# Kernel tuning notes

Hardware: AMD Instinct MI355X
Metric: run time of the kernel (lower is better)

The kernel has to match this reference:

```python
import jax, jax.numpy as jnp
import numpy as np

# Reference for Net.get_seed_aff_x4 (+ Sinkhorn), the custom-kernel hotspot of this
# module. The ResNet50 conv stack / side convs are standard cuDNN-covered ops and the
# external `resnet50` module is not part of this source; `feature` here is hie_fea
# (768ch at side3 resolution) and `norm_cam` is the bg-augmented CAM at the same
# resolution, exactly as they arrive at get_seed_aff_x4 in forward.

N, C, H, W, CF = 8, 21, 64, 64, 768
NUM_CLUSTERS = 2
KMEANS_ITERS = 10      # deterministic Lloyd iterations (external kmeans_pytorch is
                       # randomly initialized; we use first-two-valid-pixel init)
EPS_OT = 0.1
SINK_MAX_ITER = 100
SINK_THRESH = 0.01


def setup_inputs() -> dict:
    key = jax.random.key(0)
    k1, k2, k3 = jax.random.split(key, 3)
    norm_cam = jax.random.uniform(k1, (N, C, H, W), dtype=jnp.float32)
    label = (jax.random.uniform(k2, (N, C, 1, 1)) < 0.8).astype(jnp.float32)
    label = label.at[:, 0].set(1.0)  # background always present
    feature = jax.random.normal(k3, (N, CF, H, W), dtype=jnp.float32)
    return {"norm_cam": norm_cam, "label": label, "feature": feature}


def _kmeans_cosine(feat, feat_n, mask):
    # feat: [HW, CF] raw features, feat_n: [HW, CF] l2-normalized, mask: [HW] in {0,1}
    valid = mask > 0
    cnt = valid.sum()
    order = jnp.argsort(jnp.where(valid, 0, 1))  # stable: valid pixels first
    init = feat[order[:NUM_CLUSTERS]] * mask[order[:NUM_CLUSTERS], None]

    def step(centers, _):
        cn = centers / jnp.maximum(
            jnp.linalg.norm(centers, axis=-1, keepdims=True), 1e-8)
        sim = feat_n @ cn.T                                  # [HW, K]
        assign = jnp.argmax(sim, axis=-1)
        oh = jax.nn.one_hot(assign, NUM_CLUSTERS, dtype=feat.dtype) * mask[:, None]
        counts = oh.sum(0)
        new_c = (oh.T @ feat) / jnp.maximum(counts, 1.0)[:, None]
        return new_c, None

    centers, _ = jax.lax.scan(step, init, None, length=KMEANS_ITERS)
    # original `continue` when < num_clusters valid pixels -> centers stay zero
    return jnp.where(cnt >= NUM_CLUSTERS, centers, jnp.zeros_like(centers))


def _sinkhorn(K, u, v):
    # K: [C, M, Nk]; faithful to Net.Sinkhorn incl. early stop on mean |r - r0|
    def cond(state):
        i, r, c, err = state
        return (i < SINK_MAX_ITER) & (err >= SINK_THRESH)

    def body(state):
        i, r, c, _ = state
        r0 = r
        r = u / jnp.einsum('cmk,ck->cm', K, c)
        c = v / jnp.einsum('cmk,cm->ck', K, r)
        err = jnp.abs(r - r0).mean()
        return (i + 1, r, c, err)

    state0 = (jnp.int32(0), jnp.ones_like(u), jnp.ones_like(v),
              jnp.asarray(jnp.inf, u.dtype))
    _, r, c, _ = jax.lax.while_loop(cond, body, state0)
    return r[..., None] * c[..., None, :] * K


def reference(norm_cam, label, feature):
    n, c, h, w = norm_cam.shape
    cf = feature.shape[1]
    hw = h * w

    # seeds: one-hot argmax of norm_cam, gated by image-level labels
    belonging = jnp.argmax(norm_cam, axis=1)                       # [n,h,w]
    seeds = jnp.transpose(jax.nn.one_hot(belonging, c, dtype=norm_cam.dtype),
                          (0, 3, 1, 2)) * label                    # [n,c,h,w]
    # nearest-interp to feature size is identity (same HxW by construction)
    mask = seeds.reshape(n, c, hw)                                 # [n,c,hw]

    feat = feature.reshape(n, cf, hw).transpose(0, 2, 1)           # [n,hw,cf]
    feat_n = feat / jnp.maximum(
        jnp.linalg.norm(feat, axis=-1, keepdims=True), 1e-8)

    # per-(image, class) cosine k-means, fully vectorized (no python data loops)
    centers = jax.vmap(
        lambda f, fn, ms: jax.vmap(_kmeans_cosine, in_axes=(None, None, 0))(f, fn, ms)
    )(feat, feat_n, mask)                                          # [n,c,K,cf]
    cnt = (mask > 0).sum(-1)                                       # [n,c]

    # cosine similarity of ALL pixels to the 2 centers, mean over clusters
    centers_n = centers / jnp.maximum(
        jnp.linalg.norm(centers, axis=-1, keepdims=True), 1e-8)
    cos = jnp.einsum('nmd,nckd->nckm', feat_n, centers_n)          # [n,c,K,hw]
    cam = jnp.where((cnt >= NUM_CLUSTERS)[..., None],
                    cos.mean(axis=2), 0.0).reshape(n, c, h, w)

    # --- Sinkhorn OT refinement (torch.no_grad in original) ---
    feat_ot = feat / (jnp.linalg.norm(feat, axis=-1, keepdims=True) + 1e-5)
    cflat = centers.reshape(n, c * NUM_CLUSTERS, cf)
    cflat = cflat / (jnp.linalg.norm(cflat, axis=-1, keepdims=True) + 1e-5)
    sim = jnp.einsum('nmd,njd->nmj', feat_ot, cflat)               # [n,hw,c*K]
    # faithful to original's sim.view(M, N, n_cls).permute(2, 0, 1)
    sim = sim.reshape(n, hw, NUM_CLUSTERS, c).transpose(0, 3, 1, 2)  # [n,c,hw,K]
    Kmat = jax.lax.stop_gradient(jnp.exp(-(1.0 - sim) / EPS_OT))
    u = jnp.full((c, hw), 1.0 / hw, dtype=sim.dtype)
    v = jnp.full((c, NUM_CLUSTERS), 1.0 / NUM_CLUSTERS, dtype=sim.dtype)
    T = jax.vmap(lambda Kb: _sinkhorn(Kb, u, v))(Kmat)             # [n,c,hw,K]
    T = T.transpose(0, 1, 3, 2).reshape(n, c, NUM_CLUSTERS, h, w)

    # all_cam_maps.mean(dim=2) * label, then per-map max normalization
    out = cam * label
    out = out / (out.max(axis=(2, 3), keepdims=True) + 1e-5)
    return out, T


if __name__ == '__main__':
    o = reference(**setup_inputs())
    print(o[0].shape, o[1].shape)
```

## Files before the change

### kernel.cpp

```cpp
#include <hip/hip_runtime.h>
#include <hip/hip_bf16.h>
#include <stdint.h>

#define NIMG 8
#define NCLS 21
#define HW   4096
#define CF   768
#define NK   2
#define NJ   42
#define NJP  48
#define SINK_MAX 100

using uint32 = unsigned int;
using u16    = unsigned short;

__device__ __forceinline__ float b2f(u16 u){ union{uint32 i; float f;} x; x.i=((uint32)u)<<16; return x.f; }
__device__ __forceinline__ u16 f2b(float f){ union{float f; uint32 i;} x; x.f=f; return (u16)((x.i + 0x7fffu + ((x.i>>16)&1u))>>16); }

template<int BF>
__device__ __forceinline__ float ldin(const void* p, size_t idx){
    if (BF) return b2f(((const u16*)p)[idx]);
    return ((const float*)p)[idx];
}
template<int BF>
__device__ __forceinline__ void stout(void* p, size_t idx, float v){
    if (BF) ((u16*)p)[idx] = f2b(v);
    else    ((float*)p)[idx] = v;
}

__global__ void k_detect(const void* feat, int* flag){
    __shared__ int cnt;
    if (threadIdx.x == 0) cnt = 0;
    __syncthreads();
    const u16* f = (const u16*)feat;
    int bad = 0;
    for (int i = threadIdx.x; i < 4096; i += 256){
        int ex = (f[i] >> 7) & 0xFF;
        if (ex >= 160) bad++;
    }
    atomicAdd(&cnt, bad);
    __syncthreads();
    if (threadIdx.x == 0) *flag = (cnt < 64) ? 1 : 0;
}

template<int BF>
__global__ void k_seeds(const void* __restrict__ cam, const void* __restrict__ label,
                        int* __restrict__ pix_cls, const int* __restrict__ dflag){
    if (*dflag != BF) return;
    int g = blockIdx.x*256 + threadIdx.x;
    int n = g >> 12, p = g & 4095;
    float best = -1e30f; int bel = 0;
    for (int c = 0; c < NCLS; c++){
        float v = ldin<BF>(cam, (size_t)(n*NCLS + c)*HW + p);
        if (v > best){ best = v; bel = c; }
    }
    pix_cls[g] = (ldin<BF>(label, n*NCLS + bel) > 0.f) ? bel : -1;
}

template<int BF>
__global__ void k_norms(const void* __restrict__ feat, float* __restrict__ inv_n,
                        float* __restrict__ inv_ot, const int* __restrict__ dflag){
    if (*dflag != BF) return;
    int g = blockIdx.x*256 + threadIdx.x;
    int n = g >> 12, p = g & 4095;
    double s = 0.0;
    for (int k = 0; k < CF; k++){
        double v = (double)ldin<BF>(feat, (size_t)(n*CF + k)*HW + p);
        s += v*v;
    }
    double nr = sqrt(s);
    inv_n [g] = (float)(1.0/fmax(nr, 1e-8));
    inv_ot[g] = (float)(1.0/(nr + 1e-5));
}

template<int BF>
__global__ void k_transpose(const void* __restrict__ feat, float* __restrict__ featT,
                            const int* __restrict__ dflag){
    if (*dflag != BF) return;
    __shared__ float tile[64][65];
    int b = blockIdx.x;
    int n   = b / ((CF/64)*(HW/64));
    int rem = b % ((CF/64)*(HW/64));
    int kb = (rem / (HW/64)) * 64;
    int pb = (rem % (HW/64)) * 64;
    int tx = threadIdx.x & 63, ty = threadIdx.x >> 6;
    for (int i = 0; i < 16; i++){
        int k = ty*16 + i;
        tile[tx][k] = ldin<BF>(feat, ((size_t)(n*CF + kb + k))*HW + pb + tx);
    }
    __syncthreads();
    for (int i = 0; i < 16; i++){
        int p = ty*16 + i;
        featT[((size_t)(n*HW + pb + p))*CF + kb + tx] = tile[p][tx];
    }
}

__global__ void k_scan(const int* __restrict__ pix_cls, const float* __restrict__ featT,
                       int* __restrict__ cnt, int* __restrict__ plist,
                       double* __restrict__ centers){
    int b = blockIdx.x; int n = b / NCLS, c = b % NCLS;
    int lane = threadIdx.x;
    int* lst = plist + (size_t)b*HW;
    int count = 0, i0 = -1, i1 = -1;
    for (int base = 0; base < HW; base += 64){
        int cls = pix_cls[n*HW + base + lane];
        unsigned long long m = __ballot(cls == c);
        int pos = count + __popcll(m & ((1ull<<lane) - 1ull));
        if (cls == c) lst[pos] = base + lane;
        if (i0 < 0){
            if (m){ i0 = base + __ffsll((long long)m) - 1;
                    unsigned long long m2 = m & (m-1);
                    if (m2) i1 = base + __ffsll((long long)m2) - 1; }
        } else if (i1 < 0){
            if (m) i1 = base + __ffsll((long long)m) - 1;
        }
        count += __popcll(m);
    }
    if (lane == 0) cnt[b] = count;
    double* C0 = centers + (size_t)b*NK*CF;
    if (count >= 2){
        const float* r0 = featT + (size_t)(n*HW + i0)*CF;
        const float* r1 = featT + (size_t)(n*HW + i1)*CF;
        for (int e = lane; e < CF; e += 64){ C0[e] = (double)r0[e]; C0[CF+e] = (double)r1[e]; }
    } else {
        for (int e = lane; e < CF; e += 64){ C0[e] = 0.0; C0[CF+e] = 0.0; }
    }
}

__global__ __launch_bounds__(512, 1) void k_kmeans(const int* __restrict__ cnt,
                                                   const int* __restrict__ plist,
                                                   const float* __restrict__ featT,
                                                   double* __restrict__ centers){
    int b = blockIdx.x; int n = b / NCLS;
    int m = cnt[b];
    if (m < 2) return;
    __shared__ double Cs[2][CF];
    __shared__ double red[2];
    __shared__ double invn[2];
    __shared__ unsigned char asg[HW];
    __shared__ int    lst_s[HW];
    __shared__ int chg;
    __shared__ int ck0i;
    int tid = threadIdx.x, lane = tid & 63;
    const int* lst = plist + (size_t)b*HW;
    double* Cg = centers + (size_t)b*NK*CF;
    const float* fbase = featT + (size_t)n*HW*CF;
    for (int j = tid; j < CF; j += 512){ Cs[0][j] = Cg[j]; Cs[1][j] = Cg[CF+j]; }
    for (int i = tid; i < m; i += 512){ asg[i] = 255; lst_s[i] = lst[i]; }
    __syncthreads();

    for (int it = 0; it < 10; it++){
        if (tid < 2) red[tid] = 0.0;
        if (tid == 0){ chg = 0; ck0i = 0; }
        __syncthreads();
        double q0 = 0.0, q1 = 0.0;
        for (int j = tid; j < CF; j += 512){ q0 += Cs[0][j]*Cs[0][j]; q1 += Cs[1][j]*Cs[1][j]; }
        #pragma unroll
        for (int off = 32; off; off >>= 1){ q0 += __shfl_xor(q0, off); q1 += __shfl_xor(q1, off); }
        if (lane == 0){ atomicAdd(&red[0], q0); atomicAdd(&red[1], q1); }
        __syncthreads();
        if (tid == 0){
            invn[0] = 1.0/fmax(sqrt(red[0]), 1e-8);
            invn[1] = 1.0/fmax(sqrt(red[1]), 1e-8);
        }
        __syncthreads();
        double ic0 = invn[0], ic1 = invn[1];

        int myC0 = 0, myChg = 0;
        for (int l = tid; l < m; l += 512){
            const float* row = fbase + (size_t)lst_s[l]*CF;
            double s0a=0.0,s0b=0.0,s0c=0.0,s0d=0.0;
            double s1a=0.0,s1b=0.0,s1c=0.0,s1d=0.0;
            #pragma unroll 8
            for (int k = 0; k < CF; k += 4){
                float4 f = *(const float4*)(row + k);
                const double* c0 = &Cs[0][k];
                const double* c1 = &Cs[1][k];
                s0a += (double)f.x*c0[0]; s0b += (double)f.y*c0[1];
                s0c += (double)f.z*c0[2]; s0d += (double)f.w*c0[3];
                s1a += (double)f.x*c1[0]; s1b += (double)f.y*c1[1];
                s1c += (double)f.z*c1[2]; s1d += (double)f.w*c1[3];
            }
            double d0 = (s0a+s0b)+(s0c+s0d);
            double d1 = (s1a+s1b)+(s1c+s1d);
            int a = (d0*ic0 >= d1*ic1) ? 0 : 1;
            if (a == 0) myC0++;
            if (asg[l] != (unsigned char)a){ myChg++; asg[l] = (unsigned char)a; }
        }
        #pragma unroll
        for (int off = 32; off; off >>= 1){
            myC0  += __shfl_xor(myC0,  off);
            myChg += __shfl_xor(myChg, off);
        }
        if (lane == 0){
            if (myC0)  atomicAdd(&ck0i, myC0);
            if (myChg) atomicAdd(&chg,  myChg);
        }
        __syncthreads();
        if (chg == 0) break;
        int c0tot = ck0i;
        double dv0 = fmax((double)c0tot, 1.0);
        double dv1 = fmax((double)(m - c0tot), 1.0);

        float a00 = 0.f, a01 = 0.f, a10 = 0.f, a11 = 0.f;
        #pragma unroll 4
        for (int p = 0; p < m; p++){
            const float* r = fbase + (size_t)lst_s[p]*CF;
            int aa = asg[p];
            float v0 = r[tid];
            float v1 = (tid < 256) ? r[512 + tid] : 0.f;
            if (aa == 0){ a00 += v0; a01 += v1; }
            else        { a10 += v0; a11 += v1; }
        }
        Cs[0][tid] = (double)a00/dv0;
        Cs[1][tid] = (double)a10/dv1;
        if (tid < 256){
            Cs[0][512 + tid] = (double)a01/dv0;
            Cs[1][512 + tid] = (double)a11/dv1;
        }
        __syncthreads();
    }
    for (int j = tid; j < CF; j += 512){ Cg[j] = Cs[0][j]; Cg[CF+j] = Cs[1][j]; }
}

__global__ void k_invc(const double* __restrict__ centers, float* __restrict__ invc_cam,
                       float* __restrict__ invc_ot){
    int b = blockIdx.x;
    int lane = threadIdx.x;
    const double* C = centers + (size_t)b*CF;
    double s = 0.0;
    for (int e = lane; e < CF; e += 64) s += C[e]*C[e];
    for (int off = 32; off; off >>= 1) s += __shfl_xor(s, off);
    if (lane == 0){
        double nr = sqrt(s);
        invc_cam[b] = (float)(1.0/fmax(nr, 1e-8));
        invc_ot[b]  = (float)(1.0/(nr + 1e-5));
    }
}

__global__ void k_cf32(const double* __restrict__ centers, float* __restrict__ Cf32){
    int n = blockIdx.x; int tid = threadIdx.x;
    for (int idx = tid; idx < NJP*CF; idx += 256){
        int j = idx / CF, e = idx - j*CF;
        float v = (j < NJ) ? (float)centers[((size_t)n*NJ + j)*CF + e] : 0.f;
        Cf32[(size_t)n*NJP*CF + idx] = v;
    }
}

__global__ __launch_bounds__(256) void k_gemmf(const float* __restrict__ featT,
                                               const float* __restrict__ Cf32,
                                               float* __restrict__ D){
    __shared__ float Fs[128][66];
    int b = blockIdx.x; int n = b >> 6; int pbase = (b & 63)*64;
    int tid = threadIdx.x, p = tid & 63;
    int jb = __builtin_amdgcn_readfirstlane((tid >> 6)*12);
    float acc[12];
    #pragma unroll
    for (int j = 0; j < 12; j++) acc[j] = 0.f;
    for (int kc = 0; kc < CF; kc += 128){
        __syncthreads();
        for (int idx = tid; idx < 64*64; idx += 256){
            int pp = idx >> 6, cw = idx & 63;
            float2 wv = *(const float2*)(featT + (size_t)(n*HW + pbase + pp)*CF + kc + cw*2);
            Fs[cw*2    ][pp] = wv.x;
            Fs[cw*2 + 1][pp] = wv.y;
        }
        __syncthreads();
        const float* Cb = Cf32 + (size_t)n*NJP*CF + kc;
        for (int k8 = 0; k8 < 128; k8 += 8){
            #pragma unroll
            for (int j = 0; j < 12; j++){
                const float* cr = Cb + (size_t)(jb + j)*CF + k8;
                #pragma unroll
                for (int k = 0; k < 8; k++)
                    acc[j] += Fs[k8 + k][p] * cr[k];
            }
        }
    }
    float* dp = D + ((size_t)(n*HW + pbase + p))*NJP + jb;
    #pragma unroll
    for (int j = 0; j < 12; j++) dp[j] = acc[j];
}

template<int BF>
__global__ __launch_bounds__(256) void k_out0(const float* __restrict__ D,
                                              const float* __restrict__ inv_n,
                                              const float* __restrict__ invc_cam,
                                              const int* __restrict__ cnt,
                                              void* __restrict__ out0,
                                              const int* __restrict__ dflag){
    if (*dflag != BF) return;
    int b = blockIdx.x; int n = b / NCLS, c = b % NCLS;
    __shared__ float wmax[4]; __shared__ float sden;
    int tid = threadIdx.x, lane = tid & 63, w = tid >> 6;
    size_t obase = (size_t)b*HW;
    if (cnt[b] < 2){
        for (int p = tid; p < HW; p += 256) stout<BF>(out0, obase + p, 0.f);
        return;
    }
    float ic0 = invc_cam[n*NJ + 2*c], ic1 = invc_cam[n*NJ + 2*c + 1];
    const float* Dn = D + (size_t)n*HW*NJP;
    float mx = -1e30f;
    for (int p = tid; p < HW; p += 256){
        const float* dp = Dn + (size_t)p*NJP + 2*c;
        float camv = 0.5f*(dp[0]*ic0 + dp[1]*ic1)*inv_n[n*HW + p];
        mx = fmaxf(mx, camv);
    }
    for (int off = 32; off; off >>= 1) mx = fmaxf(mx, __shfl_xor(mx, off));
    if (lane == 0) wmax[w] = mx;
    __syncthreads();
    if (tid == 0) sden = fmaxf(fmaxf(wmax[0], wmax[1]), fmaxf(wmax[2], wmax[3])) + 1e-5f;
    __syncthreads();
    float den = sden;
    for (int p = tid; p < HW; p += 256){
        const float* dp = Dn + (size_t)p*NJP + 2*c;
        float camv = 0.5f*(dp[0]*ic0 + dp[1]*ic1)*inv_n[n*HW + p];
        stout<BF>(out0, obase + p, camv/den);
    }
}

__global__ void k_kmat(const float* __restrict__ D, const float* __restrict__ inv_ot,
                       const float* __restrict__ invc_ot, float* __restrict__ Kg,
                       float* __restrict__ errg, int* __restrict__ arrv){
    if (blockIdx.x == 0){
        for (int i = threadIdx.x; i < NIMG*(SINK_MAX+1); i += 256){ errg[i] = 0.f; arrv[i] = 0; }
    }
    int g = blockIdx.x*256 + threadIdx.x;
    int n = g / (NCLS*HW);
    int rem = g - n*(NCLS*HW);
    int c = rem >> 12, p = rem & 4095;
    const float* dp = D + ((size_t)n*HW + p)*NJP;
    float io = inv_ot[n*HW + p];
    float s0 = dp[c]      * io * invc_ot[n*NJ + c];
    float s1 = dp[21 + c] * io * invc_ot[n*NJ + 21 + c];
    Kg[(size_t)g*2 + 0] = expf((s0 - 1.f)*10.f);
    Kg[(size_t)g*2 + 1] = expf((s1 - 1.f)*10.f);
}

template<int BF>
__global__ __launch_bounds__(256) void k_sink(const float* __restrict__ Kg,
                                              float* __restrict__ errg,
                                              int* __restrict__ arrv,
                                              void* __restrict__ d_out,
                                              const int* __restrict__ dflag){
    if (*dflag != BF) return;
    __shared__ float K0s[HW]; __shared__ float K1s[HW]; __shared__ float rs[HW];
    __shared__ float wred[4][3]; __shared__ float sh[3];
    int b = blockIdx.x; int n = b / NCLS;
    int tid = threadIdx.x, lane = tid & 63, w = tid >> 6;
    const float* Kb = Kg + (size_t)b*HW*2;
    for (int p = tid; p < HW; p += 256){ K0s[p] = Kb[p*2]; K1s[p] = Kb[p*2+1]; rs[p] = 1.f; }
    float cc0 = 1.f, cc1 = 1.f, err = 1e30f;
    const float u = 1.f/4096.f;
    int iter = 0;
    __syncthreads();
    while (iter < SINK_MAX && err >= 0.01f){
        float p0 = 0.f, p1 = 0.f, es = 0.f;
        for (int p = tid; p < HW; p += 256){
            float k0 = K0s[p], k1 = K1s[p];
            float rn = u / (k0*cc0 + k1*cc1);
            es += fabsf(rn - rs[p]);
            rs[p] = rn;
            p0 += k0*rn; p1 += k1*rn;
        }
        #pragma unroll
        for (int off = 32; off; off >>= 1){
            p0 += __shfl_xor(p0, off); p1 += __shfl_xor(p1, off); es += __shfl_xor(es, off);
        }
        if (lane == 0){ wred[w][0] = p0; wred[w][1] = p1; wred[w][2] = es; }
        __syncthreads();
        if (tid == 0){
            float P0 = wred[0][0]+wred[1][0]+wred[2][0]+wred[3][0];
            float P1 = wred[0][1]+wred[1][1]+wred[2][1]+wred[3][1];
            float ES = wred[0][2]+wred[1][2]+wred[2][2]+wred[3][2];
            sh[0] = 0.5f/P0; sh[1] = 0.5f/P1;
            int slot = n*(SINK_MAX+1) + iter;
            atomicAdd(&errg[slot], ES);
            __threadfence();
            atomicAdd(&arrv[slot], 1);
            while (__hip_atomic_load(&arrv[slot], __ATOMIC_ACQUIRE, __HIP_MEMORY_SCOPE_AGENT) < NCLS)
                __builtin_amdgcn_s_sleep(8);
            sh[2] = __hip_atomic_load(&errg[slot], __ATOMIC_RELAXED, __HIP_MEMORY_SCOPE_AGENT)
                    * (1.f/((float)NCLS*HW));
        }
        __syncthreads();
        cc0 = sh[0]; cc1 = sh[1]; err = sh[2];
        iter++;
    }
    size_t o1 = (size_t)NIMG*NCLS*HW + (size_t)b*NK*HW;
    for (int p = tid; p < HW; p += 256){
        float rv = rs[p];
        stout<BF>(d_out, o1 + p,      rv*cc0*K0s[p]);
        stout<BF>(d_out, o1 + HW + p, rv*cc1*K1s[p]);
    }
}

extern "C" void kernel_launch(void* const* d_in, const int* in_sizes, int n_in,
                              void* d_out, int out_size, void* d_ws, size_t ws_size,
                              hipStream_t stream){
    const void* cam   = d_in[0];
    const void* label = d_in[1];
    const void* feat  = d_in[2];

    char* ws = (char*)d_ws; size_t off = 0;
    auto alloc = [&](size_t bytes)->char*{
        char* p = ws + off; off = (off + bytes + 255) & ~(size_t)255; return p;
    };
    int*    dflag    = (int*)   alloc(4);
    float*  featT    = (float*) alloc((size_t)NIMG*HW*CF*4);
    double* centers  = (double*)alloc((size_t)NIMG*NCLS*NK*CF*8);
    float*  Cf32     = (float*) alloc((size_t)NIMG*NJP*CF*4);
    float*  inv_n    = (float*) alloc((size_t)NIMG*HW*4);
    float*  inv_ot   = (float*) alloc((size_t)NIMG*HW*4);
    int*    pix_cls  = (int*)   alloc((size_t)NIMG*HW*4);
    int*    cnt      = (int*)   alloc((size_t)NIMG*NCLS*4);
    int*    plist    = (int*)   alloc((size_t)NIMG*NCLS*HW*4);
    float*  invc_cam = (float*) alloc((size_t)NIMG*NJ*4);
    float*  invc_ot  = (float*) alloc((size_t)NIMG*NJ*4);
    float*  D        = (float*) alloc((size_t)NIMG*HW*NJP*4);
    float*  Kg       = (float*) alloc((size_t)NIMG*NCLS*HW*NK*4);
    float*  errg     = (float*) alloc((size_t)NIMG*(SINK_MAX+1)*4);
    int*    arrv     = (int*)   alloc((size_t)NIMG*(SINK_MAX+1)*4);

    k_detect<<<1, 256, 0, stream>>>(feat, dflag);

    k_seeds<1><<<NIMG*HW/256, 256, 0, stream>>>(cam, label, pix_cls, dflag);
    k_seeds<0><<<NIMG*HW/256, 256, 0, stream>>>(cam, label, pix_cls, dflag);
    k_norms<1><<<NIMG*HW/256, 256, 0, stream>>>(feat, inv_n, inv_ot, dflag);
    k_norms<0><<<NIMG*HW/256, 256, 0, stream>>>(feat, inv_n, inv_ot, dflag);
    k_transpose<1><<<NIMG*(CF/64)*(HW/64), 256, 0, stream>>>(feat, featT, dflag);
    k_transpose<0><<<NIMG*(CF/64)*(HW/64), 256, 0, stream>>>(feat, featT, dflag);

    k_scan  <<<NIMG*NCLS, 64, 0, stream>>>(pix_cls, featT, cnt, plist, centers);
    k_kmeans<<<NIMG*NCLS, 512, 0, stream>>>(cnt, plist, featT, centers);
    k_invc  <<<NIMG*NJ, 64, 0, stream>>>(centers, invc_cam, invc_ot);
    k_cf32  <<<NIMG, 256, 0, stream>>>(centers, Cf32);
    k_gemmf <<<NIMG*64, 256, 0, stream>>>(featT, Cf32, D);

    k_out0<1><<<NIMG*NCLS, 256, 0, stream>>>(D, inv_n, invc_cam, cnt, d_out, dflag);
    k_out0<0><<<NIMG*NCLS, 256, 0, stream>>>(D, inv_n, invc_cam, cnt, d_out, dflag);

    k_kmat  <<<NIMG*NCLS*HW/256, 256, 0, stream>>>(D, inv_ot, invc_ot, Kg, errg, arrv);

    k_sink<1><<<NIMG*NCLS, 256, 0, stream>>>(Kg, errg, arrv, d_out, dflag);
    k_sink<0><<<NIMG*NCLS, 256, 0, stream>>>(Kg, errg, arrv, d_out, dflag);
}
```

Measured before the change: 728.0 us.

## Update k-means centroid sums incrementally from changed assignments only

Instead of re-summing every valid pixel's feature row into the centroid accumulators each iteration, the k-means kernel records the pixels whose assignment changed in a shared list and applies add/subtract deltas to persistent float sums in shared memory. This removes the full pass over all member rows per iteration, which becomes a pass over only the changed rows, batched 16 at a time for memory-level parallelism. The inner dot-product unroll is also raised. In exchange it uses more shared memory, adds shared atomics for list insertion, and accumulates in a different float order, which could shift near-tie assignments.

Measured after the change: 751.7 us. 3.3% more time.

```diff
diff --git a/kernel.cpp b/kernel.cpp
--- a/kernel.cpp
+++ b/kernel.cpp
@@ -135,23 +135,24 @@
     int m = cnt[b];
     if (m < 2) return;
     __shared__ double Cs[2][CF];
+    __shared__ float  A0[CF], A1[CF];
     __shared__ double red[2];
     __shared__ double invn[2];
     __shared__ unsigned char asg[HW];
     __shared__ int    lst_s[HW];
-    __shared__ int chg;
-    __shared__ int ck0i;
+    __shared__ int    chglist[HW];
+    __shared__ int    nchg_s, ck0i;
     int tid = threadIdx.x, lane = tid & 63;
     const int* lst = plist + (size_t)b*HW;
     double* Cg = centers + (size_t)b*NK*CF;
     const float* fbase = featT + (size_t)n*HW*CF;
-    for (int j = tid; j < CF; j += 512){ Cs[0][j] = Cg[j]; Cs[1][j] = Cg[CF+j]; }
+    for (int j = tid; j < CF; j += 512){ Cs[0][j] = Cg[j]; Cs[1][j] = Cg[CF+j]; A0[j] = 0.f; A1[j] = 0.f; }
     for (int i = tid; i < m; i += 512){ asg[i] = 255; lst_s[i] = lst[i]; }
     __syncthreads();
 
     for (int it = 0; it < 10; it++){
         if (tid < 2) red[tid] = 0.0;
-        if (tid == 0){ chg = 0; ck0i = 0; }
+        if (tid == 0){ nchg_s = 0; ck0i = 0; }
         __syncthreads();
         double q0 = 0.0, q1 = 0.0;
         for (int j = tid; j < CF; j += 512){ q0 += Cs[0][j]*Cs[0][j]; q1 += Cs[1][j]*Cs[1][j]; }
@@ -166,12 +167,12 @@
         __syncthreads();
         double ic0 = invn[0], ic1 = invn[1];
 
-        int myC0 = 0, myChg = 0;
+        int myC0 = 0;
         for (int l = tid; l < m; l += 512){
             const float* row = fbase + (size_t)lst_s[l]*CF;
             double s0a=0.0,s0b=0.0,s0c=0.0,s0d=0.0;
             double s1a=0.0,s1b=0.0,s1c=0.0,s1d=0.0;
-            #pragma unroll 8
+            #pragma unroll 16
             for (int k = 0; k < CF; k += 4){
                 float4 f = *(const float4*)(row + k);
                 const double* c0 = &Cs[0][k];
@@ -185,38 +186,63 @@
             double d1 = (s1a+s1b)+(s1c+s1d);
             int a = (d0*ic0 >= d1*ic1) ? 0 : 1;
             if (a == 0) myC0++;
-            if (asg[l] != (unsigned char)a){ myChg++; asg[l] = (unsigned char)a; }
+            unsigned char old = asg[l];
+            if (old != (unsigned char)a){
+                int wi = (old != 255) ? 1 : 0;
+                int pos = atomicAdd(&nchg_s, 1);
+                chglist[pos] = l | (a << 12) | (wi << 13);
+                asg[l] = (unsigned char)a;
+            }
         }
         #pragma unroll
-        for (int off = 32; off; off >>= 1){
-            myC0  += __shfl_xor(myC0,  off);
-            myChg += __shfl_xor(myChg, off);
-        }
-        if (lane == 0){
-            if (myC0)  atomicAdd(&ck0i, myC0);
-            if (myChg) atomicAdd(&chg,  myChg);
-        }
-        __syncthreads();
-        if (chg == 0) break;
+        for (int off = 32; off; off >>= 1) myC0 += __shfl_xor(myC0, off);
+        if (lane == 0 && myC0) atomicAdd(&ck0i, myC0);
+        __syncthreads();
+        int nc = nchg_s;
+        if (nc == 0) break;
         int c0tot = ck0i;
         double dv0 = fmax((double)c0tot, 1.0);
         double dv1 = fmax((double)(m - c0tot), 1.0);
 
-        float a00 = 0.f, a01 = 0.f, a10 = 0.f, a11 = 0.f;
-        #pragma unroll 4
-        for (int p = 0; p < m; p++){
-            const float* r = fbase + (size_t)lst_s[p]*CF;
-            int aa = asg[p];
-            float v0 = r[tid];
-            float v1 = (tid < 256) ? r[512 + tid] : 0.f;
-            if (aa == 0){ a00 += v0; a01 += v1; }
-            else        { a10 += v0; a11 += v1; }
-        }
-        Cs[0][tid] = (double)a00/dv0;
-        Cs[1][tid] = (double)a10/dv1;
-        if (tid < 256){
-            Cs[0][512 + tid] = (double)a01/dv0;
-            Cs[1][512 + tid] = (double)a11/dv1;
+        float d00 = 0.f, d01 = 0.f, d10 = 0.f, d11 = 0.f;
+        for (int base = 0; base < nc; base += 16){
+            int lim = nc - base; if (lim > 16) lim = 16;
+            float v0[16], v1[16]; int cd[16];
+            #pragma unroll
+            for (int q = 0; q < 16; q++){
+                if (q < lim){
+                    int e = chglist[base + q];
+                    cd[q] = e;
+                    const float* r = fbase + (size_t)lst_s[e & 4095]*CF;
+                    v0[q] = r[tid];
+                    v1[q] = (tid < 256) ? r[512 + tid] : 0.f;
+                }
+            }
+            #pragma unroll
+            for (int q = 0; q < 16; q++){
+                if (q < lim){
+                    int nw = (cd[q] >> 12) & 1, wi = (cd[q] >> 13) & 1;
+                    if (nw == 0){
+                        d00 += v0[q]; d01 += v1[q];
+                        if (wi){ d10 -= v0[q]; d11 -= v1[q]; }
+                    } else {
+                        d10 += v0[q]; d11 += v1[q];
+                        if (wi){ d00 -= v0[q]; d01 -= v1[q]; }
+                    }
+                }
+            }
+        }
+        {
+            float na0 = A0[tid] + d00, na1 = A1[tid] + d10;
+            A0[tid] = na0; A1[tid] = na1;
+            Cs[0][tid] = (double)na0/dv0;
+            Cs[1][tid] = (double)na1/dv1;
+            if (tid < 256){
+                float nb0 = A0[512 + tid] + d01, nb1 = A1[512 + tid] + d11;
+                A0[512 + tid] = nb0; A1[512 + tid] = nb1;
+                Cs[0][512 + tid] = (double)nb0/dv0;
+                Cs[1][512 + tid] = (double)nb1/dv1;
+            }
         }
         __syncthreads();
     }
```

## Replace pixel-major transpose with class-grouped channel-major packing for k-means

Applied to the files above, without the earlier changes.

Drops the full pixel-major transpose of the features. Instead it builds a per-image pixel index grouped by seed class and packs the features channel-major in that order, so each k-means block reads a contiguous pixel range per channel, giving coalesced loads in both the distance pass and the centroid update. The similarity GEMM now reads the original NCHW features directly. The pack kernel does a gather over the original features, which could cost more than the transpose if the accesses scatter.

Result: slower. 1.149 ms (+57.8%).

```diff
diff --git a/kernel.cpp b/kernel.cpp
--- a/kernel.cpp
+++ b/kernel.cpp
@@ -73,63 +73,57 @@
     inv_ot[g] = (float)(1.0/(nr + 1e-5));
 }
 
-template<int BF>
-__global__ void k_transpose(const void* __restrict__ feat, float* __restrict__ featT,
-                            const int* __restrict__ dflag){
-    if (*dflag != BF) return;
-    __shared__ float tile[64][65];
-    int b = blockIdx.x;
-    int n   = b / ((CF/64)*(HW/64));
-    int rem = b % ((CF/64)*(HW/64));
-    int kb = (rem / (HW/64)) * 64;
-    int pb = (rem % (HW/64)) * 64;
-    int tx = threadIdx.x & 63, ty = threadIdx.x >> 6;
-    for (int i = 0; i < 16; i++){
-        int k = ty*16 + i;
-        tile[tx][k] = ldin<BF>(feat, ((size_t)(n*CF + kb + k))*HW + pb + tx);
-    }
-    __syncthreads();
-    for (int i = 0; i < 16; i++){
-        int p = ty*16 + i;
-        featT[((size_t)(n*HW + pb + p))*CF + kb + tx] = tile[p][tx];
-    }
-}
-
-__global__ void k_scan(const int* __restrict__ pix_cls, const float* __restrict__ featT,
+__global__ void k_scan(const int* __restrict__ pix_cls,
                        int* __restrict__ cnt, int* __restrict__ plist,
                        double* __restrict__ centers){
     int b = blockIdx.x; int n = b / NCLS, c = b % NCLS;
     int lane = threadIdx.x;
     int* lst = plist + (size_t)b*HW;
-    int count = 0, i0 = -1, i1 = -1;
+    int count = 0;
     for (int base = 0; base < HW; base += 64){
         int cls = pix_cls[n*HW + base + lane];
         unsigned long long m = __ballot(cls == c);
         int pos = count + __popcll(m & ((1ull<<lane) - 1ull));
         if (cls == c) lst[pos] = base + lane;
-        if (i0 < 0){
-            if (m){ i0 = base + __ffsll((long long)m) - 1;
-                    unsigned long long m2 = m & (m-1);
-                    if (m2) i1 = base + __ffsll((long long)m2) - 1; }
-        } else if (i1 < 0){
-            if (m) i1 = base + __ffsll((long long)m) - 1;
-        }
         count += __popcll(m);
     }
     if (lane == 0) cnt[b] = count;
-    double* C0 = centers + (size_t)b*NK*CF;
-    if (count >= 2){
-        const float* r0 = featT + (size_t)(n*HW + i0)*CF;
-        const float* r1 = featT + (size_t)(n*HW + i1)*CF;
-        for (int e = lane; e < CF; e += 64){ C0[e] = (double)r0[e]; C0[CF+e] = (double)r1[e]; }
-    } else {
+    if (count < 2){
+        double* C0 = centers + (size_t)b*NK*CF;
         for (int e = lane; e < CF; e += 64){ C0[e] = 0.0; C0[CF+e] = 0.0; }
     }
 }
 
+__global__ void k_pidx(const int* __restrict__ cnt, const int* __restrict__ plist,
+                       int* __restrict__ cstartg, int* __restrict__ pidx){
+    int b = blockIdx.x; int n = b / NCLS, c = b % NCLS;
+    int lane = threadIdx.x;
+    int cbase = 0;
+    for (int cc = 0; cc < c; cc++) cbase += cnt[n*NCLS + cc];
+    if (lane == 0) cstartg[b] = cbase;
+    int m = cnt[b];
+    for (int i = lane; i < m; i += 64)
+        pidx[n*HW + cbase + i] = plist[(size_t)b*HW + i];
+}
+
+template<int BF>
+__global__ void k_pack(const void* __restrict__ feat, const int* __restrict__ pidx,
+                       const int* __restrict__ cnt, const int* __restrict__ cstartg,
+                       float* __restrict__ featCT, const int* __restrict__ dflag){
+    if (*dflag != BF) return;
+    int g = blockIdx.x*256 + threadIdx.x;
+    int n = g / (CF*HW);
+    int rem = g - n*(CF*HW);
+    int k = rem >> 12;
+    int pos = rem & 4095;
+    int tot = cstartg[n*NCLS + NCLS-1] + cnt[n*NCLS + NCLS-1];
+    if (pos < tot)
+        featCT[(size_t)g] = ldin<BF>(feat, (size_t)(n*CF + k)*HW + pidx[n*HW + pos]);
+}
+
 __global__ __launch_bounds__(512, 1) void k_kmeans(const int* __restrict__ cnt,
-                                                   const int* __restrict__ plist,
-                                                   const float* __restrict__ featT,
+                                                   const int* __restrict__ cstartg,
+                                                   const float* __restrict__ featCT,
                                                    double* __restrict__ centers){
     int b = blockIdx.x; int n = b / NCLS;
     int m = cnt[b];
@@ -138,15 +132,16 @@
     __shared__ double red[2];
     __shared__ double invn[2];
     __shared__ unsigned char asg[HW];
-    __shared__ int    lst_s[HW];
-    __shared__ int chg;
-    __shared__ int ck0i;
+    __shared__ int chg, ck0i;
     int tid = threadIdx.x, lane = tid & 63;
-    const int* lst = plist + (size_t)b*HW;
+    int cbase = cstartg[b];
     double* Cg = centers + (size_t)b*NK*CF;
-    const float* fbase = featT + (size_t)n*HW*CF;
-    for (int j = tid; j < CF; j += 512){ Cs[0][j] = Cg[j]; Cs[1][j] = Cg[CF+j]; }
-    for (int i = tid; i < m; i += 512){ asg[i] = 255; lst_s[i] = lst[i]; }
+    const float* F = featCT + (size_t)n*CF*HW;
+    for (int j = tid; j < CF; j += 512){
+        Cs[0][j] = (double)F[(size_t)j*HW + cbase];
+        Cs[1][j] = (double)F[(size_t)j*HW + cbase + 1];
+    }
+    for (int i = tid; i < m; i += 512) asg[i] = 255;
     __syncthreads();
 
     for (int it = 0; it < 10; it++){
@@ -168,18 +163,19 @@
 
         int myC0 = 0, myChg = 0;
         for (int l = tid; l < m; l += 512){
-            const float* row = fbase + (size_t)lst_s[l]*CF;
+            const float* col = F + cbase + l;
             double s0a=0.0,s0b=0.0,s0c=0.0,s0d=0.0;
             double s1a=0.0,s1b=0.0,s1c=0.0,s1d=0.0;
-            #pragma unroll 8
+            #pragma unroll 4
             for (int k = 0; k < CF; k += 4){
-                float4 f = *(const float4*)(row + k);
-                const double* c0 = &Cs[0][k];
-                const double* c1 = &Cs[1][k];
-                s0a += (double)f.x*c0[0]; s0b += (double)f.y*c0[1];
-                s0c += (double)f.z*c0[2]; s0d += (double)f.w*c0[3];
-                s1a += (double)f.x*c1[0]; s1b += (double)f.y*c1[1];
-                s1c += (double)f.z*c1[2]; s1d += (double)f.w*c1[3];
+                float f0 = col[(size_t)(k+0)*HW];
+                float f1 = col[(size_t)(k+1)*HW];
+                float f2 = col[(size_t)(k+2)*HW];
+                float f3 = col[(size_t)(k+3)*HW];
+                s0a += (double)f0*Cs[0][k+0]; s0b += (double)f1*Cs[0][k+1];
+                s0c += (double)f2*Cs[0][k+2]; s0d += (double)f3*Cs[0][k+3];
+                s1a += (double)f0*Cs[1][k+0]; s1b += (double)f1*Cs[1][k+1];
+                s1c += (double)f2*Cs[1][k+2]; s1d += (double)f3*Cs[1][k+3];
             }
             double d0 = (s0a+s0b)+(s0c+s0d);
             double d1 = (s1a+s1b)+(s1c+s1d);
@@ -202,21 +198,24 @@
         double dv0 = fmax((double)c0tot, 1.0);
         double dv1 = fmax((double)(m - c0tot), 1.0);
 
-        float a00 = 0.f, a01 = 0.f, a10 = 0.f, a11 = 0.f;
-        #pragma unroll 4
-        for (int p = 0; p < m; p++){
-            const float* r = fbase + (size_t)lst_s[p]*CF;
-            int aa = asg[p];
-            float v0 = r[tid];
-            float v1 = (tid < 256) ? r[512 + tid] : 0.f;
-            if (aa == 0){ a00 += v0; a01 += v1; }
-            else        { a10 += v0; a11 += v1; }
-        }
-        Cs[0][tid] = (double)a00/dv0;
-        Cs[1][tid] = (double)a10/dv1;
-        if (tid < 256){
-            Cs[0][512 + tid] = (double)a01/dv0;
-            Cs[1][512 + tid] = (double)a11/dv1;
+        {
+            const float* r0 = F + (size_t)tid*HW + cbase;
+            const float* r1 = F + (size_t)(512 + tid)*HW + cbase;
+            float a00 = 0.f, a01 = 0.f, a10 = 0.f, a11 = 0.f;
+            #pragma unroll 8
+            for (int i = 0; i < m; i++){
+                int aa = asg[i];
+                float v0 = r0[i];
+                float v1 = (tid < 256) ? r1[i] : 0.f;
+                if (aa == 0){ a00 += v0; a01 += v1; }
+                else        { a10 += v0; a11 += v1; }
+            }
+            Cs[0][tid] = (double)a00/dv0;
+            Cs[1][tid] = (double)a10/dv1;
+            if (tid < 256){
+                Cs[0][512 + tid] = (double)a01/dv0;
+                Cs[1][512 + tid] = (double)a11/dv1;
+            }
         }
         __syncthreads();
     }
@@ -247,9 +246,12 @@
     }
 }
 
-__global__ __launch_bounds__(256) void k_gemmf(const float* __restrict__ featT,
+template<int BF>
+__global__ __launch_bounds__(256) void k_gemmf(const void* __restrict__ feat,
                                                const float* __restrict__ Cf32,
-                                               float* __restrict__ D){
+                                               float* __restrict__ D,
+                                               const int* __restrict__ dflag){
+    if (*dflag != BF) return;
     __shared__ float Fs[128][66];
     int b = blockIdx.x; int n = b >> 6; int pbase = (b & 63)*64;
     int tid = threadIdx.x, p = tid & 63;
@@ -259,11 +261,9 @@
     for (int j = 0; j < 12; j++) acc[j] = 0.f;
     for (int kc = 0; kc < CF; kc += 128){
         __syncthreads();
-        for (int idx = tid; idx < 64*64; idx += 256){
-            int pp = idx >> 6, cw = idx & 63;
-            float2 wv = *(const float2*)(featT + (size_t)(n*HW + pbase + pp)*CF + kc + cw*2);
-            Fs[cw*2    ][pp] = wv.x;
-            Fs[cw*2 + 1][pp] = wv.y;
+        for (int idx = tid; idx < 128*64; idx += 256){
+            int kk = idx >> 6, pp = idx & 63;
+            Fs[kk][pp] = ldin<BF>(feat, (size_t)(n*CF + kc + kk)*HW + pbase + pp);
         }
         __syncthreads();
         const float* Cb = Cf32 + (size_t)n*NJP*CF + kc;
@@ -407,7 +407,7 @@
         char* p = ws + off; off = (off + bytes + 255) & ~(size_t)255; return p;
     };
     int*    dflag    = (int*)   alloc(4);
-    float*  featT    = (float*) alloc((size_t)NIMG*HW*CF*4);
+    float*  featCT   = (float*) alloc((size_t)NIMG*HW*CF*4);
     double* centers  = (double*)alloc((size_t)NIMG*NCLS*NK*CF*8);
     float*  Cf32     = (float*) alloc((size_t)NIMG*NJP*CF*4);
     float*  inv_n    = (float*) alloc((size_t)NIMG*HW*4);
@@ -415,6 +415,8 @@
     int*    pix_cls  = (int*)   alloc((size_t)NIMG*HW*4);
     int*    cnt      = (int*)   alloc((size_t)NIMG*NCLS*4);
     int*    plist    = (int*)   alloc((size_t)NIMG*NCLS*HW*4);
+    int*    pidx     = (int*)   alloc((size_t)NIMG*HW*4);
+    int*    cstartg  = (int*)   alloc((size_t)NIMG*NCLS*4);
     float*  invc_cam = (float*) alloc((size_t)NIMG*NJ*4);
     float*  invc_ot  = (float*) alloc((size_t)NIMG*NJ*4);
     float*  D        = (float*) alloc((size_t)NIMG*HW*NJP*4);
@@ -428,14 +430,18 @@
     k_seeds<0><<<NIMG*HW/256, 256, 0, stream>>>(cam, label, pix_cls, dflag);
     k_norms<1><<<NIMG*HW/256, 256, 0, stream>>>(feat, inv_n, inv_ot, dflag);
     k_norms<0><<<NIMG*HW/256, 256, 0, stream>>>(feat, inv_n, inv_ot, dflag);
-    k_transpose<1><<<NIMG*(CF/64)*(HW/64), 256, 0, stream>>>(feat, featT, dflag);
-    k_transpose<0><<<NIMG*(CF/64)*(HW/64), 256, 0, stream>>>(feat, featT, dflag);
-
-    k_scan  <<<NIMG*NCLS, 64, 0, stream>>>(pix_cls, featT, cnt, plist, centers);
-    k_kmeans<<<NIMG*NCLS, 512, 0, stream>>>(cnt, plist, featT, centers);
+
+    k_scan  <<<NIMG*NCLS, 64, 0, stream>>>(pix_cls, cnt, plist, centers);
+    k_pidx  <<<NIMG*NCLS, 64, 0, stream>>>(cnt, plist, cstartg, pidx);
+    k_pack<1><<<NIMG*CF*HW/256, 256, 0, stream>>>(feat, pidx, cnt, cstartg, featCT, dflag);
+    k_pack<0><<<NIMG*CF*HW/256, 256, 0, stream>>>(feat, pidx, cnt, cstartg, featCT, dflag);
+
+    k_kmeans<<<NIMG*NCLS, 512, 0, stream>>>(cnt, cstartg, featCT, centers);
     k_invc  <<<NIMG*NJ, 64, 0, stream>>>(centers, invc_cam, invc_ot);
     k_cf32  <<<NIMG, 256, 0, stream>>>(centers, Cf32);
-    k_gemmf <<<NIMG*64, 256, 0, stream>>>(featT, Cf32, D);
+
+    k_gemmf<1><<<NIMG*64, 256, 0, stream>>>(feat, Cf32, D, dflag);
+    k_gemmf<0><<<NIMG*64, 256, 0, stream>>>(feat, Cf32, D, dflag);
 
     k_out0<1><<<NIMG*NCLS, 256, 0, stream>>>(D, inv_n, invc_cam, cnt, d_out, dflag);
     k_out0<0><<<NIMG*NCLS, 256, 0, stream>>>(D, inv_n, invc_cam, cnt, d_out, dflag);
```
